# Optimization experiments

Hardware: AMD Instinct MI355X
Metric: run time of the kernel (lower is better)

The kernel has to match this reference:

```python
import jax, jax.numpy as jnp
import numpy as np

TAU = 2.0       # LIF time constant
ALPHA = 4.0     # spikingjelly Sigmoid surrogate alpha
EPS = 1e-5      # BatchNorm eps
NUM_HEADS = 8

@jax.custom_vjp
def _spike(x):
    return (x >= 0.0).astype(x.dtype)

def _spike_fwd(x):
    return _spike(x), x

def _spike_bwd(x, g):
    s = jax.nn.sigmoid(ALPHA * x)
    return (g * ALPHA * s * (1.0 - s),)

_spike.defvjp(_spike_fwd, _spike_bwd)

def lif(x, v_th=1.0):
    """Multi-step LIF over leading time axis. v <- v + (x - v)/tau; hard reset to 0.
    detach_reset=True: spike in reset path is stop-gradient'ed."""
    def step(v, xt):
        v = v + (xt - v) / TAU
        s = _spike(v - v_th)
        v = v * (1.0 - jax.lax.stop_gradient(s))
        return v, s
    _, out = jax.lax.scan(step, jnp.zeros_like(x[0]), x)
    return out

def conv_bn(x, w, gamma, beta, mean, var, bias=None):
    """1x1 Conv1d over channel dim + BatchNorm1d (inference-style, running stats).
    x: [T,B,C,N], w: [Cout,Cin]."""
    y = jnp.einsum('tbcn,dc->tbdn', x, w)
    if bias is not None:
        y = y + bias[None, None, :, None]
    inv = gamma * jax.lax.rsqrt(var + EPS)
    return (y - mean[None, None, :, None]) * inv[None, None, :, None] + beta[None, None, :, None]

def _bn_params(key, C):
    k1, k2, k3 = jax.random.split(key, 3)
    gamma = 1.0 + 0.1 * jax.random.normal(k1, (C,), jnp.float32)
    beta = 0.1 * jax.random.normal(k2, (C,), jnp.float32)
    mean = 0.1 * jax.random.normal(k3, (C,), jnp.float32)
    var = jnp.ones((C,), jnp.float32)
    return gamma, beta, mean, var

def setup_inputs() -> dict:
    key = jax.random.key(0)
    ks = jax.random.split(key, 10)
    T, B, C, N = 4, 8, 512, 1024
    scale = 1.0 / np.sqrt(C)
    d = {}
    d['q'] = jax.random.normal(ks[0], (T, B, C, N), jnp.float32)
    d['k'] = jax.random.normal(ks[1], (T, B, C, N), jnp.float32)
    d['q_w'] = jax.random.normal(ks[2], (C, C), jnp.float32) * scale
    d['k_w'] = jax.random.normal(ks[3], (C, C), jnp.float32) * scale
    d['proj_w'] = jax.random.normal(ks[4], (C, C), jnp.float32) * scale
    d['proj_b'] = 0.01 * jax.random.normal(ks[5], (C,), jnp.float32)
    d['q_gamma'], d['q_beta'], d['q_mean'], d['q_var'] = _bn_params(ks[6], C)
    d['k_gamma'], d['k_beta'], d['k_mean'], d['k_var'] = _bn_params(ks[7], C)
    d['proj_gamma'], d['proj_beta'], d['proj_mean'], d['proj_var'] = _bn_params(ks[8], C)
    return d

def reference(q, k, q_w, k_w, proj_w, proj_b,
              q_gamma, q_beta, q_mean, q_var,
              k_gamma, k_beta, k_mean, k_var,
              proj_gamma, proj_beta, proj_mean, proj_var):
    T, B, C, N = q.shape
    H = NUM_HEADS
    Dh = C // H
    # Q path: conv1x1 + BN + LIF spikes, split heads
    q_s = lif(conv_bn(q, q_w, q_gamma, q_beta, q_mean, q_var))          # [T,B,C,N]
    q_h = q_s.reshape(T, B, H, Dh, N)
    # K path
    k_s = lif(conv_bn(k, k_w, k_gamma, k_beta, k_mean, k_var))          # [T,B,C,N]
    k_h = k_s.reshape(T, B, H, Dh, N)
    # Sum-pool Q over head_dim, spike-gate (threshold 0.5), multiply into K
    q_sum = jnp.sum(q_h, axis=3, keepdims=True)                         # [T,B,H,1,N]
    attn = lif(q_sum, v_th=0.5)                                         # [T,B,H,1,N]
    x = (attn * k_h).reshape(T, B, C, N)
    # Projection: conv1x1 (with bias) + BN + LIF
    x = conv_bn(x, proj_w, proj_gamma, proj_beta, proj_mean, proj_var, bias=proj_b)
    return lif(x)
```

## Files before the change

### kernel.cpp

```cpp
#include <hip/hip_runtime.h>
#include <hip/hip_fp16.h>
#include <stdint.h>

#define TT 4
#define BB 8
#define CC 512
#define NN 1024
#define HH 8

typedef unsigned char u8;
typedef _Float16 f16x8 __attribute__((ext_vector_type(8)));
typedef float f32x16 __attribute__((ext_vector_type(16)));

#define WF_BYTES ((size_t)2*64*512*16)
#define SZ_SPIKE ((size_t)TT*BB*CC*NN)
#define SZ_GATE  ((size_t)TT*BB*HH*NN)

union U4H { uint4 u; f16x8 v; };
__device__ __forceinline__ f16x8 ash(uint4 u){ U4H x; x.u = u; return x.v; }

#define MFMA_F16(a,b,c) __builtin_amdgcn_mfma_f32_32x32x16_f16((a),(b),(c),0,0,0)

__device__ __forceinline__ void gld_lds4(const void* g, void* l){
  __builtin_amdgcn_global_load_lds((const __attribute__((address_space(1))) void*)g,
                                   (__attribute__((address_space(3))) void*)l, 4, 0, 0);
}

#define WAITVM(N) asm volatile("s_waitcnt vmcnt(" #N ")" ::: "memory")
#define WAITLGKM0 asm volatile("s_waitcnt lgkmcnt(0)" ::: "memory")
#define SBAR() __builtin_amdgcn_s_barrier()
#define VMFENCE() asm volatile("" ::: "memory")

__device__ __forceinline__ void split16(float xs, uint32_t& h, uint32_t& m){
  __half hh = __float2half(xs);
  float hf = __half2float(hh);
  __half mm = __float2half(xs - hf);
  h = __half_as_ushort(hh);
  m = __half_as_ushort(mm);
}

__global__ __launch_bounds__(256)
void k_prep(const float* __restrict__ W0, const float* __restrict__ W1,
            const float* __restrict__ W2,
            u8* __restrict__ D0, u8* __restrict__ D1, u8* __restrict__ D2)
{
  const int which = blockIdx.y;
  const float* W = (which == 0) ? W0 : (which == 1) ? W1 : W2;
  u8* D = (which == 0) ? D0 : (which == 1) ? D1 : D2;
  const int tg  = blockIdx.x * 256 + threadIdx.x;
  const int row = tg >> 6;
  const int kh  = tg & 63;
  uint32_t Hw[4], Mw[4];
#pragma unroll
  for (int p = 0; p < 4; ++p){
    uint32_t h0, m0, h1, m1;
    split16(W[row * CC + kh * 8 + 2*p    ] * 64.0f, h0, m0);
    split16(W[row * CC + kh * 8 + 2*p + 1] * 64.0f, h1, m1);
    Hw[p] = h0 | (h1 << 16);
    Mw[p] = m0 | (m1 << 16);
  }
  *(uint4*)(D + ((size_t)(0*64 + kh)*512 + row) * 16) = make_uint4(Hw[0],Hw[1],Hw[2],Hw[3]);
  *(uint4*)(D + ((size_t)(1*64 + kh)*512 + row) * 16) = make_uint4(Mw[0],Mw[1],Mw[2],Mw[3]);
}

__global__ __launch_bounds__(256, 2)
void k_qk(const float* __restrict__ Q, const float* __restrict__ K,
          const u8* __restrict__ WFq, const u8* __restrict__ WFk,
          const float* __restrict__ qg, const float* __restrict__ qb,
          const float* __restrict__ qm, const float* __restrict__ qv,
          const float* __restrict__ kg, const float* __restrict__ kb,
          const float* __restrict__ km, const float* __restrict__ kv,
          u8* __restrict__ Sk, u8* __restrict__ Aa)
{
  __shared__ uint4 frag[2][1024];

  const int hw = blockIdx.x;
  const int lg = (hw & 7) * 128 + (hw >> 3);
  const int d0t  = lg & 1;
  const int n0i  = (lg >> 1) & 31;
  const int b    = (lg >> 6) & 7;
  const int path = (lg >> 9) & 1;
  const int n0 = n0i << 5, d0 = d0t << 8;
  const float* X = path ? K : Q;
  const u8* WF = path ? WFk : WFq;

  const int tid = threadIdx.x, lane = tid & 63, wid = tid >> 6;
  const int hi = lane >> 5, ln31 = lane & 31;

  const int c  = tid & 127;
  const int kq = tid >> 7;
  const int ct_t = c >> 5, nn = c & 31;
  const float* Xb = X + ((size_t)(ct_t*BB + b)*CC)*NN + n0 + nn;

  f32x16 acc[4][2];
#pragma unroll
  for (int i = 0; i < 4; ++i)
#pragma unroll
    for (int j = 0; j < 2; ++j)
#pragma unroll
      for (int r = 0; r < 16; ++r) acc[i][j][r] = 0.0f;

  uint4 A[8];
  float xb[2][16];

  auto loadA = [&](int H){
#pragma unroll
    for (int s = 0; s < 2; ++s)
#pragma unroll
      for (int ks = 0; ks < 2; ++ks)
#pragma unroll
        for (int rt = 0; rt < 2; ++rt)
          A[(s*2 + ks)*2 + rt] = *(const uint4*)(WF +
              ((size_t)(s*64 + H*4 + ks*2 + hi)*512
               + d0 + wid*64 + rt*32 + ln31) * 16);
  };
  auto loadX = [&](int ktile, float* xr){
    const float* xp = Xb + (size_t)(ktile*32 + kq*16)*NN;
#pragma unroll
    for (int j = 0; j < 16; ++j) xr[j] = xp[(size_t)j*NN];
  };
  auto split_write = [&](const float* xr, int fb){
    uint32_t hw_[8], mw_[8];
#pragma unroll
    for (int p = 0; p < 8; ++p){
      uint32_t ha, ma, hb2, mb2;
      split16(xr[2*p    ] * 512.0f, ha, ma);
      split16(xr[2*p + 1] * 512.0f, hb2, mb2);
      hw_[p] = ha | (hb2 << 16);
      mw_[p] = ma | (mb2 << 16);
    }
    frag[fb][(kq*2    )*128 + c] = make_uint4(hw_[0],hw_[1],hw_[2],hw_[3]);
    frag[fb][(kq*2 + 1)*128 + c] = make_uint4(hw_[4],hw_[5],hw_[6],hw_[7]);
    frag[fb][(4 + kq*2    )*128 + c] = make_uint4(mw_[0],mw_[1],mw_[2],mw_[3]);
    frag[fb][(4 + kq*2 + 1)*128 + c] = make_uint4(mw_[4],mw_[5],mw_[6],mw_[7]);
  };
  auto mstep = [&](int fb){
#pragma unroll
    for (int ks = 0; ks < 2; ++ks){
      const int kbi = ks*2 + hi;
#pragma unroll
      for (int ct = 0; ct < 4; ++ct){
        f16x8 bh = ash(frag[fb][kbi*128 + ct*32 + ln31]);
        f16x8 bm = ash(frag[fb][(4 + kbi)*128 + ct*32 + ln31]);
#pragma unroll
        for (int rt = 0; rt < 2; ++rt){
          acc[ct][rt] = MFMA_F16(ash(A[(0*2 + ks)*2 + rt]), bh, acc[ct][rt]);
          acc[ct][rt] = MFMA_F16(ash(A[(1*2 + ks)*2 + rt]), bh, acc[ct][rt]);
          acc[ct][rt] = MFMA_F16(ash(A[(0*2 + ks)*2 + rt]), bm, acc[ct][rt]);
        }
      }
    }
  };

#define QK_PH(H, XL, XN, FC, FN) { \
    loadA(H); VMFENCE(); \
    loadX((H)+2, xb[XN]); VMFENCE(); \
    split_write(xb[XL], FN); \
    mstep(FC); \
    WAITLGKM0; SBAR(); }

  loadX(0, xb[0]); VMFENCE();
  loadX(1, xb[1]); VMFENCE();
  split_write(xb[0], 0);
  WAITLGKM0; SBAR();

  for (int Hb = 0; Hb < 14; Hb += 2){
    QK_PH(Hb,     1, 0, 0, 1)
    QK_PH(Hb + 1, 0, 1, 1, 0)
  }
  { loadA(14); VMFENCE(); split_write(xb[1], 1); mstep(0); WAITLGKM0; SBAR(); }
  { loadA(15); VMFENCE(); mstep(1); }
#undef QK_PH

  const float* gamma = path ? kg : qg;
  const float* beta  = path ? kb : qb;
  const float* mean  = path ? km : qm;
  const float* var   = path ? kv : qv;

  uint32_t orb = 0;
#pragma unroll
  for (int rt = 0; rt < 2; ++rt)
#pragma unroll
    for (int rg = 0; rg < 4; ++rg){
      const int dbase = d0 + wid*64 + rt*32 + rg*8 + hi*4;
      const float4 g4 = *(const float4*)&gamma[dbase];
      const float4 b4 = *(const float4*)&beta[dbase];
      const float4 m4 = *(const float4*)&mean[dbase];
      const float4 v4 = *(const float4*)&var[dbase];
      const float* gp = (const float*)&g4;
      const float* bp = (const float*)&b4;
      const float* mp = (const float*)&m4;
      const float* vp = (const float*)&v4;
#pragma unroll
      for (int j = 0; j < 4; ++j){
        const float inv = gp[j] * (1.0f / sqrtf(vp[j] + 1e-5f));
        const float c1 = inv * (1.0f/32768.0f);
        const float c0 = bp[j] - mp[j]*inv;
        const int r = rg*4 + j;
        float v = 0.f;
#pragma unroll
        for (int t = 0; t < 4; ++t){
          const float y = fmaf(acc[t][rt][r], c1, c0);
          v = 0.5f*(v + y);
          const bool s = (v >= 1.0f);
          if (s) v = 0.f;
          if (path == 1)
            Sk[((size_t)(t*BB + b)*CC + dbase + j)*NN + n0 + ln31] = (u8)s;
          else
            orb |= ((uint32_t)s) << t;
        }
      }
    }

  if (path == 0){
    orb |= __shfl_xor(orb, 32);
    if (hi == 0){
      const int h = d0t*4 + wid;
#pragma unroll
      for (int t = 0; t < 4; ++t)
        Aa[((size_t)(t*BB + b)*HH + h)*NN + n0 + ln31] = (u8)((orb >> t) & 1);
    }
  }
}

__global__ __launch_bounds__(256, 2)
void k_proj(const u8* __restrict__ Sk, const u8* __restrict__ Ag,
            const u8* __restrict__ WF, const float* __restrict__ bias,
            const float* __restrict__ gamma, const float* __restrict__ beta,
            const float* __restrict__ mean, const float* __restrict__ var,
            float* __restrict__ O)
{
  __shared__ u8   xu[3][8192];
  __shared__ uint4 frag[1024];

  const int hw = blockIdx.x;
  const int lg = (hw & 7) * 64 + (hw >> 3);
  const int d0t = lg & 1;
  const int n0i = (lg >> 1) & 31;
  const int b   = (lg >> 6) & 7;
  const int n0 = n0i << 5, d0 = d0t << 8;

  const int tid = threadIdx.x, lane = tid & 63, wid = tid >> 6;
  const int hi = lane >> 5, ln31 = lane & 31;

  const int st_kh = tid >> 5, st_t = (tid >> 3) & 3, st_n4 = tid & 7;

  f32x16 acc[4][2];
#pragma unroll
  for (int t = 0; t < 4; ++t)
#pragma unroll
    for (int rt = 0; rt < 2; ++rt)
#pragma unroll
      for (int r = 0; r < 16; ++r) acc[t][rt][r] = 0.0f;

  uint4 Ap[16];
  uint32_t gword[8];
#pragma unroll
  for (int p = 0; p < 8; ++p)
    gword[p] = *(const uint32_t*)(Ag +
        ((size_t)(st_t*BB + b)*HH + p)*NN + n0 + st_n4*4);

  auto xustage = [&](int h, int buf){
#pragma unroll
    for (int i = 0; i < 8; ++i){
      const u8* g = Sk + ((size_t)((wid*BB + b)*CC) + (size_t)(h*64 + i*8 + (lane >> 3)))*NN
                       + n0 + (lane & 7)*4;
      gld_lds4(g, (void*)&xu[buf][(wid*64 + i*8)*32]);
    }
  };
  auto loadPA = [&](int p){
#pragma unroll
    for (int s = 0; s < 2; ++s)
#pragma unroll
      for (int ks = 0; ks < 4; ++ks)
#pragma unroll
        for (int rt = 0; rt < 2; ++rt)
          Ap[(s*4 + ks)*2 + rt] = *(const uint4*)(WF +
              ((size_t)(s*64 + p*8 + ks*2 + hi)*512
               + d0 + wid*64 + rt*32 + ln31) * 16);
  };
  auto stage2 = [&](int buf, uint32_t g32){
    uint32_t r[8];
#pragma unroll
    for (int cc = 0; cc < 8; ++cc)
      r[cc] = *(const uint32_t*)&xu[buf][(st_t*64 + st_kh*8 + cc)*32 + st_n4*4];
#pragma unroll
    for (int j = 0; j < 4; ++j){
      const uint32_t gm   = __builtin_amdgcn_perm(g32, g32, (uint32_t)j * 0x01010101u);
      const uint32_t selp = (uint32_t)j | (((uint32_t)j + 4u) << 8);
      uint32_t p01 = __builtin_amdgcn_perm(r[1], r[0], selp);
      uint32_t p23 = __builtin_amdgcn_perm(r[3], r[2], selp);
      uint32_t p45 = __builtin_amdgcn_perm(r[5], r[4], selp);
      uint32_t p67 = __builtin_amdgcn_perm(r[7], r[6], selp);
      uint32_t lo  = __builtin_amdgcn_perm(p23, p01, 0x05040100u) & gm;
      uint32_t hi_ = __builtin_amdgcn_perm(p67, p45, 0x05040100u) & gm;
      uint32_t w[4];
#pragma unroll
      for (int p = 0; p < 4; ++p){
        const uint32_t src = (p < 2) ? lo : hi_;
        const uint32_t b0 = (src >> ((p & 1) * 16)) & 0xFFu;
        const uint32_t b1 = (src >> ((p & 1) * 16 + 8)) & 0xFFu;
        w[p] = (b0 ? 0x3C00u : 0u) | (b1 ? 0x3C000000u : 0u);
      }
      frag[st_kh*128 + st_t*32 + st_n4*4 + j] = make_uint4(w[0], w[1], w[2], w[3]);
    }
  };
  auto mstepP = [&](){
#pragma unroll
    for (int ks = 0; ks < 4; ++ks){
      const int kbi = ks*2 + hi;
#pragma unroll
      for (int ct = 0; ct < 4; ++ct){
        const int fb = ct*32 + ln31;
        f16x8 bb = ash(frag[kbi*128 + fb]);
#pragma unroll
        for (int rt = 0; rt < 2; ++rt){
          acc[ct][rt] = MFMA_F16(ash(Ap[(0*4 + ks)*2 + rt]), bb, acc[ct][rt]);
          acc[ct][rt] = MFMA_F16(ash(Ap[(1*4 + ks)*2 + rt]), bb, acc[ct][rt]);
        }
      }
    }
  };

#define PJ_PH(P, VM) { \
    WAITVM(VM); SBAR(); \
    loadPA(P); VMFENCE(); \
    if ((P) < 6) { xustage((P)+2, ((P)+2)%3); VMFENCE(); } \
    stage2((P)%3, gword[P]); \
    WAITLGKM0; SBAR(); \
    mstepP(); }

  xustage(0, 0); VMFENCE(); xustage(1, 1); VMFENCE();
  PJ_PH(0,8) PJ_PH(1,8) PJ_PH(2,8) PJ_PH(3,8)
  PJ_PH(4,8) PJ_PH(5,8) PJ_PH(6,8) PJ_PH(7,0)
#undef PJ_PH

#pragma unroll
  for (int rt = 0; rt < 2; ++rt)
#pragma unroll
    for (int rg = 0; rg < 4; ++rg){
      const int dbase = d0 + wid*64 + rt*32 + rg*8 + hi*4;
      const float4 g4 = *(const float4*)&gamma[dbase];
      const float4 b4 = *(const float4*)&beta[dbase];
      const float4 m4 = *(const float4*)&mean[dbase];
      const float4 v4 = *(const float4*)&var[dbase];
      const float4 s4 = *(const float4*)&bias[dbase];
      const float* gp = (const float*)&g4;
      const float* bp = (const float*)&b4;
      const float* mp = (const float*)&m4;
      const float* vp = (const float*)&v4;
      const float* sp = (const float*)&s4;
#pragma unroll
      for (int j = 0; j < 4; ++j){
        const float inv = gp[j] * (1.0f / sqrtf(vp[j] + 1e-5f));
        const float c1 = inv * (1.0f/64.0f);
        const float c0 = (sp[j] - mp[j])*inv + bp[j];
        const int r = rg*4 + j;
        float v = 0.f;
#pragma unroll
        for (int t = 0; t < 4; ++t){
          const float y = fmaf(acc[t][rt][r], c1, c0);
          v = 0.5f*(v + y);
          const bool s = (v >= 1.0f);
          if (s) v = 0.f;
          O[((size_t)(t*BB + b)*CC + dbase + j)*NN + n0 + ln31] = s ? 1.f : 0.f;
        }
      }
    }
}

extern "C" void kernel_launch(void* const* d_in, const int* in_sizes, int n_in,
                              void* d_out, int out_size, void* d_ws, size_t ws_size,
                              hipStream_t stream)
{
  const float* q   = (const float*)d_in[0];
  const float* k   = (const float*)d_in[1];
  const float* qw  = (const float*)d_in[2];
  const float* kw  = (const float*)d_in[3];
  const float* pw  = (const float*)d_in[4];
  const float* pb  = (const float*)d_in[5];
  const float* qg  = (const float*)d_in[6];
  const float* qbt = (const float*)d_in[7];
  const float* qm  = (const float*)d_in[8];
  const float* qv  = (const float*)d_in[9];
  const float* kg  = (const float*)d_in[10];
  const float* kbt = (const float*)d_in[11];
  const float* km  = (const float*)d_in[12];
  const float* kv  = (const float*)d_in[13];
  const float* pg  = (const float*)d_in[14];
  const float* pbt = (const float*)d_in[15];
  const float* pm  = (const float*)d_in[16];
  const float* pv  = (const float*)d_in[17];

  u8* WFq = (u8*)d_ws;
  u8* WFk = WFq + WF_BYTES;
  u8* WFp = WFk + WF_BYTES;
  u8* Sk  = WFp + WF_BYTES;
  u8* Aa  = Sk + SZ_SPIKE;
  const size_t need = 3*WF_BYTES + SZ_SPIKE + SZ_GATE;
  if (ws_size < need) return;

  k_prep<<<dim3(128, 3), 256, 0, stream>>>(qw, kw, pw, WFq, WFk, WFp);
  k_qk<<<1024, 256, 0, stream>>>(q, k, WFq, WFk,
                                 qg, qbt, qm, qv, kg, kbt, km, kv, Sk, Aa);
  k_proj<<<512, 256, 0, stream>>>(Sk, Aa, WFp, pb, pg, pbt, pm, pv, (float*)d_out);
}
```

Before: 164.2 us.

## Warp-specialize k_qk into MFMA consumer and X-loading producer waves

Doubles the k_qk block to 512 threads. Four waves now only run MFMAs with double-buffered weight registers and raised priority. The other four waves stream X tiles three deep, split them into f16 hi/lo pairs and write them into double-buffered LDS fragments, with block barriers keeping the two groups in step. The aim is to stop global X-load latency and split arithmetic from stalling the matrix math. The cost is more waves per block, more registers per thread, and barrier counts that must match exactly across both roles.

```diff
diff --git a/kernel.cpp b/kernel.cpp
--- a/kernel.cpp
+++ b/kernel.cpp
@@ -63,7 +63,7 @@
   *(uint4*)(D + ((size_t)(1*64 + kh)*512 + row) * 16) = make_uint4(Mw[0],Mw[1],Mw[2],Mw[3]);
 }
 
-__global__ __launch_bounds__(256, 2)
+__global__ __launch_bounds__(512, 2)
 void k_qk(const float* __restrict__ Q, const float* __restrict__ K,
           const u8* __restrict__ WFq, const u8* __restrict__ WFk,
           const float* __restrict__ qg, const float* __restrict__ qb,
@@ -84,142 +84,171 @@
   const float* X = path ? K : Q;
   const u8* WF = path ? WFk : WFq;
 
-  const int tid = threadIdx.x, lane = tid & 63, wid = tid >> 6;
+  const int tid = threadIdx.x, lane = tid & 63, wid8 = tid >> 6;
   const int hi = lane >> 5, ln31 = lane & 31;
 
-  const int c  = tid & 127;
-  const int kq = tid >> 7;
-  const int ct_t = c >> 5, nn = c & 31;
-  const float* Xb = X + ((size_t)(ct_t*BB + b)*CC)*NN + n0 + nn;
-
-  f32x16 acc[4][2];
-#pragma unroll
-  for (int i = 0; i < 4; ++i)
-#pragma unroll
-    for (int j = 0; j < 2; ++j)
-#pragma unroll
-      for (int r = 0; r < 16; ++r) acc[i][j][r] = 0.0f;
-
-  uint4 A[8];
-  float xb[2][16];
-
-  auto loadA = [&](int H){
-#pragma unroll
-    for (int s = 0; s < 2; ++s)
-#pragma unroll
-      for (int ks = 0; ks < 2; ++ks)
-#pragma unroll
-        for (int rt = 0; rt < 2; ++rt)
-          A[(s*2 + ks)*2 + rt] = *(const uint4*)(WF +
-              ((size_t)(s*64 + H*4 + ks*2 + hi)*512
-               + d0 + wid*64 + rt*32 + ln31) * 16);
-  };
-  auto loadX = [&](int ktile, float* xr){
-    const float* xp = Xb + (size_t)(ktile*32 + kq*16)*NN;
-#pragma unroll
-    for (int j = 0; j < 16; ++j) xr[j] = xp[(size_t)j*NN];
-  };
-  auto split_write = [&](const float* xr, int fb){
-    uint32_t hw_[8], mw_[8];
-#pragma unroll
-    for (int p = 0; p < 8; ++p){
-      uint32_t ha, ma, hb2, mb2;
-      split16(xr[2*p    ] * 512.0f, ha, ma);
-      split16(xr[2*p + 1] * 512.0f, hb2, mb2);
-      hw_[p] = ha | (hb2 << 16);
-      mw_[p] = ma | (mb2 << 16);
+  if (wid8 < 4){
+    const int wid = wid8;
+    f32x16 acc[4][2];
+#pragma unroll
+    for (int i = 0; i < 4; ++i)
+#pragma unroll
+      for (int j = 0; j < 2; ++j)
+#pragma unroll
+        for (int r = 0; r < 16; ++r) acc[i][j][r] = 0.0f;
+
+    uint4 A0[8], A1[8];
+    auto loadA = [&](uint4* A, int H){
+#pragma unroll
+      for (int s = 0; s < 2; ++s)
+#pragma unroll
+        for (int ks = 0; ks < 2; ++ks)
+#pragma unroll
+          for (int rt = 0; rt < 2; ++rt)
+            A[(s*2 + ks)*2 + rt] = *(const uint4*)(WF +
+                ((size_t)(s*64 + H*4 + ks*2 + hi)*512
+                 + d0 + wid*64 + rt*32 + ln31) * 16);
+    };
+    auto mstep = [&](const uint4* A, int fb){
+#pragma unroll
+      for (int ks = 0; ks < 2; ++ks){
+        const int kbi = ks*2 + hi;
+#pragma unroll
+        for (int ct = 0; ct < 4; ++ct){
+          f16x8 bh = ash(frag[fb][kbi*128 + ct*32 + ln31]);
+          f16x8 bm = ash(frag[fb][(4 + kbi)*128 + ct*32 + ln31]);
+#pragma unroll
+          for (int rt = 0; rt < 2; ++rt){
+            acc[ct][rt] = MFMA_F16(ash(A[(0*2 + ks)*2 + rt]), bh, acc[ct][rt]);
+            acc[ct][rt] = MFMA_F16(ash(A[(1*2 + ks)*2 + rt]), bh, acc[ct][rt]);
+            acc[ct][rt] = MFMA_F16(ash(A[(0*2 + ks)*2 + rt]), bm, acc[ct][rt]);
+          }
+        }
+      }
+    };
+
+    loadA(A0, 0); VMFENCE();
+    SBAR();
+
+#define C_IT(T, ACUR, ANXT, DOLOAD, VMw) { \
+      if (DOLOAD) { loadA(ANXT, (T)+1); VMFENCE(); } \
+      WAITVM(VMw); \
+      __builtin_amdgcn_s_setprio(1); \
+      mstep(ACUR, (T)&1); \
+      __builtin_amdgcn_s_setprio(0); \
+      WAITLGKM0; SBAR(); }
+
+    C_IT(0,  A0, A1, 1, 8)  C_IT(1,  A1, A0, 1, 8)
+    C_IT(2,  A0, A1, 1, 8)  C_IT(3,  A1, A0, 1, 8)
+    C_IT(4,  A0, A1, 1, 8)  C_IT(5,  A1, A0, 1, 8)
+    C_IT(6,  A0, A1, 1, 8)  C_IT(7,  A1, A0, 1, 8)
+    C_IT(8,  A0, A1, 1, 8)  C_IT(9,  A1, A0, 1, 8)
+    C_IT(10, A0, A1, 1, 8)  C_IT(11, A1, A0, 1, 8)
+    C_IT(12, A0, A1, 1, 8)  C_IT(13, A1, A0, 1, 8)
+    C_IT(14, A0, A1, 1, 8)  C_IT(15, A1, A0, 0, 0)
+#undef C_IT
+
+    const float* gamma = path ? kg : qg;
+    const float* beta  = path ? kb : qb;
+    const float* mean  = path ? km : qm;
+    const float* var   = path ? kv : qv;
+
+    uint32_t orb = 0;
+#pragma unroll
+    for (int rt = 0; rt < 2; ++rt)
+#pragma unroll
+      for (int rg = 0; rg < 4; ++rg){
+        const int dbase = d0 + wid*64 + rt*32 + rg*8 + hi*4;
+        const float4 g4 = *(const float4*)&gamma[dbase];
+        const float4 b4 = *(const float4*)&beta[dbase];
+        const float4 m4 = *(const float4*)&mean[dbase];
+        const float4 v4 = *(const float4*)&var[dbase];
+        const float* gp = (const float*)&g4;
+        const float* bp = (const float*)&b4;
+        const float* mp = (const float*)&m4;
+        const float* vp = (const float*)&v4;
+#pragma unroll
+        for (int j = 0; j < 4; ++j){
+          const float inv = gp[j] * (1.0f / sqrtf(vp[j] + 1e-5f));
+          const float c1 = inv * (1.0f/32768.0f);
+          const float c0 = bp[j] - mp[j]*inv;
+          const int r = rg*4 + j;
+          float v = 0.f;
+#pragma unroll
+          for (int t = 0; t < 4; ++t){
+            const float y = fmaf(acc[t][rt][r], c1, c0);
+            v = 0.5f*(v + y);
+            const bool s = (v >= 1.0f);
+            if (s) v = 0.f;
+            if (path == 1)
+              Sk[((size_t)(t*BB + b)*CC + dbase + j)*NN + n0 + ln31] = (u8)s;
+            else
+              orb |= ((uint32_t)s) << t;
+          }
+        }
+      }
+
+    if (path == 0){
+      orb |= __shfl_xor(orb, 32);
+      if (hi == 0){
+        const int h = d0t*4 + wid;
+#pragma unroll
+        for (int t = 0; t < 4; ++t)
+          Aa[((size_t)(t*BB + b)*HH + h)*NN + n0 + ln31] = (u8)((orb >> t) & 1);
+      }
     }
-    frag[fb][(kq*2    )*128 + c] = make_uint4(hw_[0],hw_[1],hw_[2],hw_[3]);
-    frag[fb][(kq*2 + 1)*128 + c] = make_uint4(hw_[4],hw_[5],hw_[6],hw_[7]);
-    frag[fb][(4 + kq*2    )*128 + c] = make_uint4(mw_[0],mw_[1],mw_[2],mw_[3]);
-    frag[fb][(4 + kq*2 + 1)*128 + c] = make_uint4(mw_[4],mw_[5],mw_[6],mw_[7]);
-  };
-  auto mstep = [&](int fb){
-#pragma unroll
-    for (int ks = 0; ks < 2; ++ks){
-      const int kbi = ks*2 + hi;
-#pragma unroll
-      for (int ct = 0; ct < 4; ++ct){
-        f16x8 bh = ash(frag[fb][kbi*128 + ct*32 + ln31]);
-        f16x8 bm = ash(frag[fb][(4 + kbi)*128 + ct*32 + ln31]);
-#pragma unroll
-        for (int rt = 0; rt < 2; ++rt){
-          acc[ct][rt] = MFMA_F16(ash(A[(0*2 + ks)*2 + rt]), bh, acc[ct][rt]);
-          acc[ct][rt] = MFMA_F16(ash(A[(1*2 + ks)*2 + rt]), bh, acc[ct][rt]);
-          acc[ct][rt] = MFMA_F16(ash(A[(0*2 + ks)*2 + rt]), bm, acc[ct][rt]);
-        }
-      }
-    }
-  };
-
-#define QK_PH(H, XL, XN, FC, FN) { \
-    loadA(H); VMFENCE(); \
-    loadX((H)+2, xb[XN]); VMFENCE(); \
-    split_write(xb[XL], FN); \
-    mstep(FC); \
-    WAITLGKM0; SBAR(); }
-
-  loadX(0, xb[0]); VMFENCE();
-  loadX(1, xb[1]); VMFENCE();
-  split_write(xb[0], 0);
-  WAITLGKM0; SBAR();
-
-  for (int Hb = 0; Hb < 14; Hb += 2){
-    QK_PH(Hb,     1, 0, 0, 1)
-    QK_PH(Hb + 1, 0, 1, 1, 0)
-  }
-  { loadA(14); VMFENCE(); split_write(xb[1], 1); mstep(0); WAITLGKM0; SBAR(); }
-  { loadA(15); VMFENCE(); mstep(1); }
-#undef QK_PH
-
-  const float* gamma = path ? kg : qg;
-  const float* beta  = path ? kb : qb;
-  const float* mean  = path ? km : qm;
-  const float* var   = path ? kv : qv;
-
-  uint32_t orb = 0;
-#pragma unroll
-  for (int rt = 0; rt < 2; ++rt)
-#pragma unroll
-    for (int rg = 0; rg < 4; ++rg){
-      const int dbase = d0 + wid*64 + rt*32 + rg*8 + hi*4;
-      const float4 g4 = *(const float4*)&gamma[dbase];
-      const float4 b4 = *(const float4*)&beta[dbase];
-      const float4 m4 = *(const float4*)&mean[dbase];
-      const float4 v4 = *(const float4*)&var[dbase];
-      const float* gp = (const float*)&g4;
-      const float* bp = (const float*)&b4;
-      const float* mp = (const float*)&m4;
-      const float* vp = (const float*)&v4;
-#pragma unroll
-      for (int j = 0; j < 4; ++j){
-        const float inv = gp[j] * (1.0f / sqrtf(vp[j] + 1e-5f));
-        const float c1 = inv * (1.0f/32768.0f);
-        const float c0 = bp[j] - mp[j]*inv;
-        const int r = rg*4 + j;
-        float v = 0.f;
-#pragma unroll
-        for (int t = 0; t < 4; ++t){
-          const float y = fmaf(acc[t][rt][r], c1, c0);
-          v = 0.5f*(v + y);
-          const bool s = (v >= 1.0f);
-          if (s) v = 0.f;
-          if (path == 1)
-            Sk[((size_t)(t*BB + b)*CC + dbase + j)*NN + n0 + ln31] = (u8)s;
-          else
-            orb |= ((uint32_t)s) << t;
-        }
-      }
-    }
-
-  if (path == 0){
-    orb |= __shfl_xor(orb, 32);
-    if (hi == 0){
-      const int h = d0t*4 + wid;
-#pragma unroll
-      for (int t = 0; t < 4; ++t)
-        Aa[((size_t)(t*BB + b)*HH + h)*NN + n0 + ln31] = (u8)((orb >> t) & 1);
-    }
+  } else {
+    const int p = wid8 - 4;
+    const float* Xb = X + ((size_t)(p*BB + b)*CC)*NN + n0 + ln31;
+
+    float xr0[16], xr1[16], xr2[16];
+    auto loadX = [&](int tile, float* xr){
+      const float* xp = Xb + (size_t)(tile*32 + hi*16)*NN;
+#pragma unroll
+      for (int j = 0; j < 16; ++j) xr[j] = xp[(size_t)j*NN];
+    };
+    auto splitw = [&](const float* xr, int fb){
+      uint32_t hw_[8], mw_[8];
+#pragma unroll
+      for (int pr = 0; pr < 8; ++pr){
+        uint32_t ha, ma, hb2, mb2;
+        split16(xr[2*pr    ] * 512.0f, ha, ma);
+        split16(xr[2*pr + 1] * 512.0f, hb2, mb2);
+        hw_[pr] = ha | (hb2 << 16);
+        mw_[pr] = ma | (mb2 << 16);
+      }
+      const int col = p*32 + ln31;
+      frag[fb][(hi*2    )*128 + col] = make_uint4(hw_[0],hw_[1],hw_[2],hw_[3]);
+      frag[fb][(hi*2 + 1)*128 + col] = make_uint4(hw_[4],hw_[5],hw_[6],hw_[7]);
+      frag[fb][(4 + hi*2    )*128 + col] = make_uint4(mw_[0],mw_[1],mw_[2],mw_[3]);
+      frag[fb][(4 + hi*2 + 1)*128 + col] = make_uint4(mw_[4],mw_[5],mw_[6],mw_[7]);
+    };
+
+    loadX(0, xr0); VMFENCE();
+    loadX(1, xr1); VMFENCE();
+    loadX(2, xr2); VMFENCE();
+    WAITVM(32);
+    splitw(xr0, 0);
+    WAITLGKM0;
+    SBAR();
+
+#define P_IT(T, XNXT, XSPL, DOLOAD, VMw) { \
+      if (DOLOAD) { loadX((T)+3, XNXT); VMFENCE(); } \
+      WAITVM(VMw); \
+      splitw(XSPL, ((T)+1)&1); \
+      WAITLGKM0; SBAR(); }
+
+    P_IT(0,  xr0, xr1, 1, 32)  P_IT(1,  xr1, xr2, 1, 32)
+    P_IT(2,  xr2, xr0, 1, 32)  P_IT(3,  xr0, xr1, 1, 32)
+    P_IT(4,  xr1, xr2, 1, 32)  P_IT(5,  xr2, xr0, 1, 32)
+    P_IT(6,  xr0, xr1, 1, 32)  P_IT(7,  xr1, xr2, 1, 32)
+    P_IT(8,  xr2, xr0, 1, 32)  P_IT(9,  xr0, xr1, 1, 32)
+    P_IT(10, xr1, xr2, 1, 32)  P_IT(11, xr2, xr0, 1, 32)
+    P_IT(12, xr0, xr1, 1, 32)
+    P_IT(13, xr0, xr2, 0, 16)
+    P_IT(14, xr0, xr0, 0, 0)
+#undef P_IT
+    SBAR();
   }
 }
 
@@ -401,7 +430,7 @@
   if (ws_size < need) return;
 
   k_prep<<<dim3(128, 3), 256, 0, stream>>>(qw, kw, pw, WFq, WFk, WFp);
-  k_qk<<<1024, 256, 0, stream>>>(q, k, WFq, WFk,
+  k_qk<<<1024, 512, 0, stream>>>(q, k, WFq, WFk,
                                  qg, qbt, qm, qv, kg, kbt, km, kv, Sk, Aa);
   k_proj<<<512, 256, 0, stream>>>(Sk, Aa, WFp, pb, pg, pbt, pm, pv, (float*)d_out);
 }
```

Measured after the change: 189.3 us. +15.3%, slower.

## Load X MFMA operands directly into registers, dropping the LDS staging in k_qk

Applied to the files above, without the earlier changes.

The Q/K projection kernel stops staging the fp16 hi/lo split of X through shared memory with barriers. Each lane now loads the X elements it needs straight from global memory, splits them in registers and feeds them to the MFMAs. Weight fragments and X are double-buffered in registers across 16-channel k-steps. This removes LDS writes, reads and block barriers, but each wave now loads X redundantly, and register pressure from the 64 float buffers may hurt occupancy.

```diff
diff --git a/kernel.cpp b/kernel.cpp
--- a/kernel.cpp
+++ b/kernel.cpp
@@ -72,8 +72,6 @@
           const float* __restrict__ km, const float* __restrict__ kv,
           u8* __restrict__ Sk, u8* __restrict__ Aa)
 {
-  __shared__ uint4 frag[2][1024];
-
   const int hw = blockIdx.x;
   const int lg = (hw & 7) * 128 + (hw >> 3);
   const int d0t  = lg & 1;
@@ -87,11 +85,6 @@
   const int tid = threadIdx.x, lane = tid & 63, wid = tid >> 6;
   const int hi = lane >> 5, ln31 = lane & 31;
 
-  const int c  = tid & 127;
-  const int kq = tid >> 7;
-  const int ct_t = c >> 5, nn = c & 31;
-  const float* Xb = X + ((size_t)(ct_t*BB + b)*CC)*NN + n0 + nn;
-
   f32x16 acc[4][2];
 #pragma unroll
   for (int i = 0; i < 4; ++i)
@@ -100,77 +93,64 @@
 #pragma unroll
       for (int r = 0; r < 16; ++r) acc[i][j][r] = 0.0f;
 
-  uint4 A[8];
-  float xb[2][16];
-
-  auto loadA = [&](int H){
+  const float* xp0 = X + ((size_t)(0*BB + b)*CC + hi*8)*NN + n0 + ln31;
+  const float* xp1 = X + ((size_t)(1*BB + b)*CC + hi*8)*NN + n0 + ln31;
+  const float* xp2 = X + ((size_t)(2*BB + b)*CC + hi*8)*NN + n0 + ln31;
+  const float* xp3 = X + ((size_t)(3*BB + b)*CC + hi*8)*NN + n0 + ln31;
+  const u8* Ab = WF + ((size_t)(d0 + wid*64 + ln31)) * 16;
+
+  auto loadX = [&](int s16, float* xr){
+#pragma unroll
+    for (int j = 0; j < 8; ++j){
+      const size_t off = (size_t)(s16*16 + j) * NN;
+      xr[0*8 + j] = xp0[off];
+      xr[1*8 + j] = xp1[off];
+      xr[2*8 + j] = xp2[off];
+      xr[3*8 + j] = xp3[off];
+    }
+  };
+  auto loadA = [&](int s16, uint4* A){
 #pragma unroll
     for (int s = 0; s < 2; ++s)
 #pragma unroll
-      for (int ks = 0; ks < 2; ++ks)
-#pragma unroll
-        for (int rt = 0; rt < 2; ++rt)
-          A[(s*2 + ks)*2 + rt] = *(const uint4*)(WF +
-              ((size_t)(s*64 + H*4 + ks*2 + hi)*512
-               + d0 + wid*64 + rt*32 + ln31) * 16);
-  };
-  auto loadX = [&](int ktile, float* xr){
-    const float* xp = Xb + (size_t)(ktile*32 + kq*16)*NN;
-#pragma unroll
-    for (int j = 0; j < 16; ++j) xr[j] = xp[(size_t)j*NN];
-  };
-  auto split_write = [&](const float* xr, int fb){
-    uint32_t hw_[8], mw_[8];
-#pragma unroll
-    for (int p = 0; p < 8; ++p){
-      uint32_t ha, ma, hb2, mb2;
-      split16(xr[2*p    ] * 512.0f, ha, ma);
-      split16(xr[2*p + 1] * 512.0f, hb2, mb2);
-      hw_[p] = ha | (hb2 << 16);
-      mw_[p] = ma | (mb2 << 16);
-    }
-    frag[fb][(kq*2    )*128 + c] = make_uint4(hw_[0],hw_[1],hw_[2],hw_[3]);
-    frag[fb][(kq*2 + 1)*128 + c] = make_uint4(hw_[4],hw_[5],hw_[6],hw_[7]);
-    frag[fb][(4 + kq*2    )*128 + c] = make_uint4(mw_[0],mw_[1],mw_[2],mw_[3]);
-    frag[fb][(4 + kq*2 + 1)*128 + c] = make_uint4(mw_[4],mw_[5],mw_[6],mw_[7]);
-  };
-  auto mstep = [&](int fb){
-#pragma unroll
-    for (int ks = 0; ks < 2; ++ks){
-      const int kbi = ks*2 + hi;
-#pragma unroll
-      for (int ct = 0; ct < 4; ++ct){
-        f16x8 bh = ash(frag[fb][kbi*128 + ct*32 + ln31]);
-        f16x8 bm = ash(frag[fb][(4 + kbi)*128 + ct*32 + ln31]);
-#pragma unroll
-        for (int rt = 0; rt < 2; ++rt){
-          acc[ct][rt] = MFMA_F16(ash(A[(0*2 + ks)*2 + rt]), bh, acc[ct][rt]);
-          acc[ct][rt] = MFMA_F16(ash(A[(1*2 + ks)*2 + rt]), bh, acc[ct][rt]);
-          acc[ct][rt] = MFMA_F16(ash(A[(0*2 + ks)*2 + rt]), bm, acc[ct][rt]);
-        }
-      }
-    }
-  };
-
-#define QK_PH(H, XL, XN, FC, FN) { \
-    loadA(H); VMFENCE(); \
-    loadX((H)+2, xb[XN]); VMFENCE(); \
-    split_write(xb[XL], FN); \
-    mstep(FC); \
-    WAITLGKM0; SBAR(); }
-
-  loadX(0, xb[0]); VMFENCE();
-  loadX(1, xb[1]); VMFENCE();
-  split_write(xb[0], 0);
-  WAITLGKM0; SBAR();
-
-  for (int Hb = 0; Hb < 14; Hb += 2){
-    QK_PH(Hb,     1, 0, 0, 1)
-    QK_PH(Hb + 1, 0, 1, 1, 0)
+      for (int rt = 0; rt < 2; ++rt)
+        A[s*2 + rt] = *(const uint4*)(Ab +
+            ((size_t)(s*64 + s16*2 + hi)*512 + rt*32) * 16);
+  };
+  auto compute = [&](const float* xr, const uint4* A){
+#pragma unroll
+    for (int ct = 0; ct < 4; ++ct){
+      uint32_t hw_[4], mw_[4];
+#pragma unroll
+      for (int p = 0; p < 4; ++p){
+        uint32_t ha, ma, hb2, mb2;
+        split16(xr[ct*8 + 2*p    ] * 512.0f, ha, ma);
+        split16(xr[ct*8 + 2*p + 1] * 512.0f, hb2, mb2);
+        hw_[p] = ha | (hb2 << 16);
+        mw_[p] = ma | (mb2 << 16);
+      }
+      const uint4 bh = make_uint4(hw_[0], hw_[1], hw_[2], hw_[3]);
+      const uint4 bm = make_uint4(mw_[0], mw_[1], mw_[2], mw_[3]);
+#pragma unroll
+      for (int rt = 0; rt < 2; ++rt){
+        acc[ct][rt] = MFMA_F16(ash(A[0*2 + rt]), ash(bh), acc[ct][rt]);
+        acc[ct][rt] = MFMA_F16(ash(A[1*2 + rt]), ash(bh), acc[ct][rt]);
+        acc[ct][rt] = MFMA_F16(ash(A[0*2 + rt]), ash(bm), acc[ct][rt]);
+      }
+    }
+  };
+
+  float x0[32], x1[32];
+  uint4 A0[4], A1[4];
+  loadX(0, x0); loadA(0, A0);
+  loadX(1, x1); loadA(1, A1);
+#pragma unroll
+  for (int sp = 0; sp < 16; ++sp){
+    compute(x0, A0);
+    if (sp < 15){ loadX(2*sp + 2, x0); loadA(2*sp + 2, A0); }
+    compute(x1, A1);
+    if (sp < 15){ loadX(2*sp + 3, x1); loadA(2*sp + 3, A1); }
   }
-  { loadA(14); VMFENCE(); split_write(xb[1], 1); mstep(0); WAITLGKM0; SBAR(); }
-  { loadA(15); VMFENCE(); mstep(1); }
-#undef QK_PH
 
   const float* gamma = path ? kg : qg;
   const float* beta  = path ? kb : qb;
```

After: 193.8 us. 1.18x slower.

## Halve k_qk output tile to raise occupancy and restructure its pipeline

Applied to the files above, without the earlier changes.

The QK GEMM kernel now gives each block a 128-wide output-channel tile instead of 256, so each wave holds one 32-row tile, the grid doubles to 2048 blocks and launch bounds allow 4 blocks per CU. The pipeline changes from double-buffered X registers to one X buffer with prefetch one k-tile ahead. The Q-path gate reduction now uses LDS atomicOr, because a head's 64 channels span two waves. The aim is higher occupancy and lower register pressure to hide latency, at the cost of loading each X tile twice (once per d-tile) and more extra syncs.

```diff
diff --git a/kernel.cpp b/kernel.cpp
--- a/kernel.cpp
+++ b/kernel.cpp
@@ -63,7 +63,7 @@
   *(uint4*)(D + ((size_t)(1*64 + kh)*512 + row) * 16) = make_uint4(Mw[0],Mw[1],Mw[2],Mw[3]);
 }
 
-__global__ __launch_bounds__(256, 2)
+__global__ __launch_bounds__(256, 4)
 void k_qk(const float* __restrict__ Q, const float* __restrict__ K,
           const u8* __restrict__ WFq, const u8* __restrict__ WFk,
           const float* __restrict__ qg, const float* __restrict__ qb,
@@ -75,12 +75,12 @@
   __shared__ uint4 frag[2][1024];
 
   const int hw = blockIdx.x;
-  const int lg = (hw & 7) * 128 + (hw >> 3);
-  const int d0t  = lg & 1;
-  const int n0i  = (lg >> 1) & 31;
-  const int b    = (lg >> 6) & 7;
-  const int path = (lg >> 9) & 1;
-  const int n0 = n0i << 5, d0 = d0t << 8;
+  const int lg = (hw & 7) * 256 + (hw >> 3);
+  const int d0t  = lg & 3;
+  const int n0i  = (lg >> 2) & 31;
+  const int b    = (lg >> 7) & 7;
+  const int path = (lg >> 10) & 1;
+  const int n0 = n0i << 5, d0 = d0t << 7;
   const float* X = path ? K : Q;
   const u8* WF = path ? WFk : WFq;
 
@@ -92,97 +92,91 @@
   const int ct_t = c >> 5, nn = c & 31;
   const float* Xb = X + ((size_t)(ct_t*BB + b)*CC)*NN + n0 + nn;
 
-  f32x16 acc[4][2];
+  f32x16 acc[4];
 #pragma unroll
   for (int i = 0; i < 4; ++i)
 #pragma unroll
-    for (int j = 0; j < 2; ++j)
-#pragma unroll
-      for (int r = 0; r < 16; ++r) acc[i][j][r] = 0.0f;
-
-  uint4 A[8];
-  float xb[2][16];
-
+    for (int r = 0; r < 16; ++r) acc[i][r] = 0.0f;
+
+  uint4 A[4];
+  float xr[16];
+
+  auto loadX = [&](int tile){
+    const float* xp = Xb + (size_t)(tile*32 + kq*16)*NN;
+#pragma unroll
+    for (int j = 0; j < 16; ++j) xr[j] = xp[(size_t)j*NN];
+  };
   auto loadA = [&](int H){
 #pragma unroll
     for (int s = 0; s < 2; ++s)
 #pragma unroll
-      for (int ks = 0; ks < 2; ++ks)
-#pragma unroll
-        for (int rt = 0; rt < 2; ++rt)
-          A[(s*2 + ks)*2 + rt] = *(const uint4*)(WF +
-              ((size_t)(s*64 + H*4 + ks*2 + hi)*512
-               + d0 + wid*64 + rt*32 + ln31) * 16);
-  };
-  auto loadX = [&](int ktile, float* xr){
-    const float* xp = Xb + (size_t)(ktile*32 + kq*16)*NN;
-#pragma unroll
-    for (int j = 0; j < 16; ++j) xr[j] = xp[(size_t)j*NN];
-  };
-  auto split_write = [&](const float* xr, int fb){
-    uint32_t hw_[8], mw_[8];
-#pragma unroll
-    for (int p = 0; p < 8; ++p){
-      uint32_t ha, ma, hb2, mb2;
-      split16(xr[2*p    ] * 512.0f, ha, ma);
-      split16(xr[2*p + 1] * 512.0f, hb2, mb2);
-      hw_[p] = ha | (hb2 << 16);
-      mw_[p] = ma | (mb2 << 16);
-    }
-    frag[fb][(kq*2    )*128 + c] = make_uint4(hw_[0],hw_[1],hw_[2],hw_[3]);
-    frag[fb][(kq*2 + 1)*128 + c] = make_uint4(hw_[4],hw_[5],hw_[6],hw_[7]);
-    frag[fb][(4 + kq*2    )*128 + c] = make_uint4(mw_[0],mw_[1],mw_[2],mw_[3]);
-    frag[fb][(4 + kq*2 + 1)*128 + c] = make_uint4(mw_[4],mw_[5],mw_[6],mw_[7]);
+      for (int ksc = 0; ksc < 2; ++ksc)
+        A[s*2 + ksc] = *(const uint4*)(WF +
+            ((size_t)(s*64 + H*4 + ksc*2 + hi)*512 + d0 + wid*32 + ln31) * 16);
+  };
+  auto split_write = [&](int fb){
+#pragma unroll
+    for (int half = 0; half < 2; ++half){
+      uint32_t hw_[4], mw_[4];
+#pragma unroll
+      for (int p = 0; p < 4; ++p){
+        uint32_t ha, ma, hb2, mb2;
+        split16(xr[half*8 + 2*p    ] * 512.0f, ha, ma);
+        split16(xr[half*8 + 2*p + 1] * 512.0f, hb2, mb2);
+        hw_[p] = ha | (hb2 << 16);
+        mw_[p] = ma | (mb2 << 16);
+      }
+      frag[fb][(    kq*2 + half)*128 + c] = make_uint4(hw_[0],hw_[1],hw_[2],hw_[3]);
+      frag[fb][(4 + kq*2 + half)*128 + c] = make_uint4(mw_[0],mw_[1],mw_[2],mw_[3]);
+    }
   };
   auto mstep = [&](int fb){
 #pragma unroll
-    for (int ks = 0; ks < 2; ++ks){
-      const int kbi = ks*2 + hi;
+    for (int ksc = 0; ksc < 2; ++ksc){
+      const int klr = ksc*2 + hi;
 #pragma unroll
       for (int ct = 0; ct < 4; ++ct){
-        f16x8 bh = ash(frag[fb][kbi*128 + ct*32 + ln31]);
-        f16x8 bm = ash(frag[fb][(4 + kbi)*128 + ct*32 + ln31]);
-#pragma unroll
-        for (int rt = 0; rt < 2; ++rt){
-          acc[ct][rt] = MFMA_F16(ash(A[(0*2 + ks)*2 + rt]), bh, acc[ct][rt]);
-          acc[ct][rt] = MFMA_F16(ash(A[(1*2 + ks)*2 + rt]), bh, acc[ct][rt]);
-          acc[ct][rt] = MFMA_F16(ash(A[(0*2 + ks)*2 + rt]), bm, acc[ct][rt]);
-        }
-      }
-    }
-  };
-
-#define QK_PH(H, XL, XN, FC, FN) { \
-    loadA(H); VMFENCE(); \
-    loadX((H)+2, xb[XN]); VMFENCE(); \
-    split_write(xb[XL], FN); \
-    mstep(FC); \
-    WAITLGKM0; SBAR(); }
-
-  loadX(0, xb[0]); VMFENCE();
-  loadX(1, xb[1]); VMFENCE();
-  split_write(xb[0], 0);
+        f16x8 bh = ash(frag[fb][klr*128 + ct*32 + ln31]);
+        f16x8 bm = ash(frag[fb][(4 + klr)*128 + ct*32 + ln31]);
+        acc[ct] = MFMA_F16(ash(A[0*2 + ksc]), bh, acc[ct]);
+        acc[ct] = MFMA_F16(ash(A[1*2 + ksc]), bh, acc[ct]);
+        acc[ct] = MFMA_F16(ash(A[0*2 + ksc]), bm, acc[ct]);
+      }
+    }
+  };
+
+  loadX(0); VMFENCE();
+  loadA(0); VMFENCE();
+  WAITVM(4);
+  split_write(0);
   WAITLGKM0; SBAR();
 
-  for (int Hb = 0; Hb < 14; Hb += 2){
-    QK_PH(Hb,     1, 0, 0, 1)
-    QK_PH(Hb + 1, 0, 1, 1, 0)
-  }
-  { loadA(14); VMFENCE(); split_write(xb[1], 1); mstep(0); WAITLGKM0; SBAR(); }
-  { loadA(15); VMFENCE(); mstep(1); }
-#undef QK_PH
+#define QK_IT(H) { \
+    if ((H) < 15) { loadX((H)+1); VMFENCE(); } \
+    mstep((H)&1); \
+    if ((H) < 15) { \
+      loadA((H)+1); VMFENCE(); \
+      WAITVM(4); \
+      split_write(((H)+1)&1); \
+      WAITLGKM0; \
+    } \
+    SBAR(); }
+
+  QK_IT(0)  QK_IT(1)  QK_IT(2)  QK_IT(3)
+  QK_IT(4)  QK_IT(5)  QK_IT(6)  QK_IT(7)
+  QK_IT(8)  QK_IT(9)  QK_IT(10) QK_IT(11)
+  QK_IT(12) QK_IT(13) QK_IT(14) QK_IT(15)
+#undef QK_IT
 
   const float* gamma = path ? kg : qg;
   const float* beta  = path ? kb : qb;
   const float* mean  = path ? km : qm;
   const float* var   = path ? kv : qv;
 
-  uint32_t orb = 0;
-#pragma unroll
-  for (int rt = 0; rt < 2; ++rt)
+  if (path == 1){
 #pragma unroll
     for (int rg = 0; rg < 4; ++rg){
-      const int dbase = d0 + wid*64 + rt*32 + rg*8 + hi*4;
+      const int dbase = d0 + wid*32 + rg*8 + hi*4;
       const float4 g4 = *(const float4*)&gamma[dbase];
       const float4 b4 = *(const float4*)&beta[dbase];
       const float4 m4 = *(const float4*)&mean[dbase];
@@ -200,25 +194,58 @@
         float v = 0.f;
 #pragma unroll
         for (int t = 0; t < 4; ++t){
-          const float y = fmaf(acc[t][rt][r], c1, c0);
+          const float y = fmaf(acc[t][r], c1, c0);
           v = 0.5f*(v + y);
           const bool s = (v >= 1.0f);
           if (s) v = 0.f;
-          if (path == 1)
-            Sk[((size_t)(t*BB + b)*CC + dbase + j)*NN + n0 + ln31] = (u8)s;
-          else
-            orb |= ((uint32_t)s) << t;
+          Sk[((size_t)(t*BB + b)*CC + dbase + j)*NN + n0 + ln31] = (u8)s;
         }
       }
     }
-
-  if (path == 0){
-    orb |= __shfl_xor(orb, 32);
-    if (hi == 0){
-      const int h = d0t*4 + wid;
-#pragma unroll
-      for (int t = 0; t < 4; ++t)
-        Aa[((size_t)(t*BB + b)*HH + h)*NN + n0 + ln31] = (u8)((orb >> t) & 1);
+  } else {
+    uint32_t orb = 0;
+#pragma unroll
+    for (int rg = 0; rg < 4; ++rg){
+      const int dbase = d0 + wid*32 + rg*8 + hi*4;
+      const float4 g4 = *(const float4*)&gamma[dbase];
+      const float4 b4 = *(const float4*)&beta[dbase];
+      const float4 m4 = *(const float4*)&mean[dbase];
+      const float4 v4 = *(const float4*)&var[dbase];
+      const float* gp = (const float*)&g4;
+      const float* bp = (const float*)&b4;
+      const float* mp = (const float*)&m4;
+      const float* vp = (const float*)&v4;
+#pragma unroll
+      for (int j = 0; j < 4; ++j){
+        const float inv = gp[j] * (1.0f / sqrtf(vp[j] + 1e-5f));
+        const float c1 = inv * (1.0f/32768.0f);
+        const float c0 = bp[j] - mp[j]*inv;
+        const int r = rg*4 + j;
+        float v = 0.f;
+#pragma unroll
+        for (int t = 0; t < 4; ++t){
+          const float y = fmaf(acc[t][r], c1, c0);
+          v = 0.5f*(v + y);
+          const bool s = (v >= 1.0f);
+          if (s) v = 0.f;
+          orb |= ((uint32_t)s) << t;
+        }
+      }
+    }
+    __syncthreads();
+    uint32_t* gw = (uint32_t*)&frag[1][0];
+    if (tid < 64) gw[tid] = 0;
+    __syncthreads();
+    const int hl2 = wid >> 1;
+#pragma unroll
+    for (int t = 0; t < 4; ++t)
+      if ((orb >> t) & 1)
+        atomicOr(&gw[hl2*32 + t*8 + (ln31 >> 2)], 1u << ((ln31 & 3)*8));
+    __syncthreads();
+    if (tid < 64){
+      const int hl = tid >> 5, t = (tid >> 3) & 3, nw = tid & 7;
+      *(uint32_t*)(Aa + ((size_t)(t*BB + b)*HH + d0t*2 + hl)*NN + n0 + nw*4) =
+          gw[hl*32 + t*8 + nw];
     }
   }
 }
@@ -401,7 +428,7 @@
   if (ws_size < need) return;
 
   k_prep<<<dim3(128, 3), 256, 0, stream>>>(qw, kw, pw, WFq, WFk, WFp);
-  k_qk<<<1024, 256, 0, stream>>>(q, k, WFq, WFk,
+  k_qk<<<2048, 256, 0, stream>>>(q, k, WFq, WFk,
                                  qg, qbt, qm, qv, kg, kbt, km, kv, Sk, Aa);
   k_proj<<<512, 256, 0, stream>>>(Sk, Aa, WFp, pb, pg, pbt, pm, pv, (float*)d_out);
 }
```

Result: no change. 166.6 us (+1.4%).
